# Kernel tuning notes

Hardware: AMD Instinct MI355X
Metric: run time of the kernel (lower is better)

## Reference

```python
import jax, jax.numpy as jnp
import numpy as np

N_TOKEN = 267735
D = 512           # d_embed == d_proj
DIV = 4
CUTS = [0, 20000, 40000, 200000, 267735]  # cutoff_ends
N_TOKENS_BATCH = 1024  # len*bsz


def setup_inputs() -> dict:
    key = jax.random.key(0)
    ks = jax.random.split(key, 16)
    inp = {}
    inp["hidden"] = jax.random.normal(ks[0], (N_TOKENS_BATCH, D), jnp.float32)
    inp["target"] = jax.random.randint(ks[1], (N_TOKENS_BATCH,), 0, N_TOKEN)
    d_embs = [D // DIV ** i for i in range(4)]          # 512, 128, 32, 8
    sizes = [CUTS[i + 1] - CUTS[i] for i in range(4)]   # 20000, 20000, 160000, 67735
    for i in range(4):
        inp[f"W{i}"] = jax.random.normal(ks[2 + 3 * i], (sizes[i], d_embs[i]), jnp.float32) * (d_embs[i] ** -0.5)
        inp[f"b{i}"] = jax.random.normal(ks[3 + 3 * i], (sizes[i],), jnp.float32) * 0.01
        inp[f"proj{i}"] = jax.random.normal(ks[4 + 3 * i], (D, d_embs[i]), jnp.float32) * (D ** -0.5)
    inp["cluster_weight"] = jax.random.normal(ks[14], (3, D), jnp.float32) * (D ** -0.5)
    inp["cluster_bias"] = jax.random.normal(ks[15], (3,), jnp.float32) * 0.01
    return inp


def reference(hidden, target, W0, b0, proj0, W1, b1, proj1, W2, b2, proj2, W3, b3, proj3, cluster_weight, cluster_bias):
    n = jnp.arange(target.shape[0])
    # head = shortlist vocab + one logit per tail cluster
    head_w = jnp.concatenate([W0, cluster_weight], axis=0)   # [20003, D]
    head_b = jnp.concatenate([b0, cluster_bias], axis=0)     # [20003]
    head_logit = (hidden @ proj0) @ head_w.T + head_b        # einsum('bd,de,ev->bv')
    head_lp = jax.nn.log_softmax(head_logit, axis=-1)        # [N, 20003]
    head_size = head_lp.shape[1]
    # cluster id per token (0 = shortlist, 1..3 = tails)
    cid = ((target >= CUTS[1]).astype(jnp.int32)
           + (target >= CUTS[2]).astype(jnp.int32)
           + (target >= CUTS[3]).astype(jnp.int32))
    # shortlist: nll = -head_logprob[n, target]
    nll = -head_lp[n, jnp.clip(target, 0, CUTS[1] - 1)]
    for i, (Wi, bi, pi) in enumerate([(W1, b1, proj1), (W2, b2, proj2), (W3, b3, proj3)], start=1):
        l, r = CUTS[i], CUTS[i + 1]
        tail_lp = jax.nn.log_softmax((hidden @ pi) @ Wi.T + bi, axis=-1)  # [N, r-l]
        rel = jnp.clip(target - l, 0, r - l - 1)
        # faithful to original: head column indexed as head_logprob[:, -i]
        lp_i = head_lp[:, head_size - i] + tail_lp[n, rel]
        nll = jnp.where(cid == i, -lp_i, nll)
    return nll
```

## Files before the change

kernel.cpp:

```cpp
#include <hip/hip_runtime.h>

typedef short s16x8 __attribute__((ext_vector_type(8)));
typedef unsigned short u16x8 __attribute__((ext_vector_type(8)));
typedef float f32x4 __attribute__((ext_vector_type(4)));
typedef unsigned short ushort;

#define NTOK 1024
#define DHID 512

#define VH   20003
#define KH   512
#define NCH_H 80
#define TPC_H 16
#define VH_PAD 20480

#define V1   20000
#define K1   128
#define NCH_1 80
#define TPC_1 16
#define V1_PAD 20480

#define V2   160000
#define K2   32
#define NCH_2 128
#define TPC_2 80
#define V2_PAD 163840

#define V3   67735
#define K3   32
#define NCH_3 67
#define TPC_3 64
#define V3_PAD 68608

#define PAD_BIAS (-1e30f)

#define OFF_HW   0UL
#define OFF_W1   (OFF_HW  + (unsigned long)VH_PAD*KH*2)
#define OFF_W2   (OFF_W1  + (unsigned long)V1_PAD*K1*2)
#define OFF_W3   (OFF_W2  + (unsigned long)V2_PAD*K2*2)
#define OFF_HID  (OFF_W3  + (unsigned long)V3_PAD*K3*2)
#define OFF_PT0  (OFF_HID + (unsigned long)NTOK*DHID*2)
#define OFF_PT1  (OFF_PT0 + (unsigned long)512*DHID*2)
#define OFF_PT2  (OFF_PT1 + (unsigned long)128*DHID*2)
#define OFF_PT3  (OFF_PT2 + (unsigned long)32*DHID*2)
#define OFF_H0   (OFF_PT3 + (unsigned long)32*DHID*2)
#define OFF_H1   (OFF_H0  + (unsigned long)NTOK*512*2)
#define OFF_H2   (OFF_H1  + (unsigned long)NTOK*128*2)
#define OFF_H3   (OFF_H2  + (unsigned long)NTOK*32*2)
#define OFF_HB   (OFF_H3  + (unsigned long)NTOK*32*2)
#define OFF_B1   (OFF_HB  + (unsigned long)VH_PAD*4)
#define OFF_B2   (OFF_B1  + (unsigned long)V1_PAD*4)
#define OFF_B3   (OFF_B2  + (unsigned long)V2_PAD*4)
#define OFF_SH   (OFF_B3  + (unsigned long)V3_PAD*4)
#define OFF_S1   (OFF_SH  + (unsigned long)NTOK*NCH_H*4)
#define OFF_S2   (OFF_S1  + (unsigned long)NTOK*NCH_1*4)
#define OFF_S3   (OFF_S2  + (unsigned long)NTOK*NCH_2*4)

__device__ __forceinline__ ushort f2bf(float f) {
    union { float f; unsigned u; } x; x.f = f;
    unsigned r = x.u + 0x7fffu + ((x.u >> 16) & 1u);
    return (ushort)(r >> 16);
}
__device__ __forceinline__ float bf2f(ushort h) {
    union { unsigned u; float f; } x; x.u = ((unsigned)h) << 16;
    return x.f;
}
__device__ __forceinline__ f32x4 mfma_bf16(s16x8 a, s16x8 b, f32x4 c) {
    return __builtin_amdgcn_mfma_f32_16x16x32_bf16(a, b, c, 0, 0, 0);
}
__device__ __forceinline__ void ld8(const float* p, float* v) {
    float4 a = *(const float4*)p, b = *(const float4*)(p + 4);
    v[0]=a.x; v[1]=a.y; v[2]=a.z; v[3]=a.w; v[4]=b.x; v[5]=b.y; v[6]=b.z; v[7]=b.w;
}

__device__ __forceinline__ void gld_lds16(const ushort* g, ushort* l) {
    __builtin_amdgcn_global_load_lds(
        (const __attribute__((address_space(1))) unsigned int*)g,
        (__attribute__((address_space(3))) unsigned int*)l, 16, 0, 0);
}

#define WB_HW  20480L
#define WB_W1  5120L
#define WB_W2  10240L
#define WB_W3  4288L
#define WB_HID 1024L
#define WB_PT0 512L
#define WB_PT1 128L
#define WB_PT2 32L
#define WB_PT3 32L
#define WB_TOTAL (WB_HW+WB_W1+WB_W2+WB_W3+WB_HID+WB_PT0+WB_PT1+WB_PT2+WB_PT3)

__global__ __launch_bounds__(256) void prep_wswz(
    const float* __restrict__ hidden,
    const float* __restrict__ W0, const float* __restrict__ cw,
    const float* __restrict__ W1, const float* __restrict__ W2, const float* __restrict__ W3,
    const float* __restrict__ p0, const float* __restrict__ p1,
    const float* __restrict__ p2, const float* __restrict__ p3,
    ushort* __restrict__ hw, ushort* __restrict__ ow1,
    ushort* __restrict__ ow2, ushort* __restrict__ ow3,
    ushort* __restrict__ hid,
    ushort* __restrict__ pT0, ushort* __restrict__ pT1,
    ushort* __restrict__ pT2, ushort* __restrict__ pT3)
{
    int lane = threadIdx.x & 63;
    int r = lane & 15, quad = lane >> 4;
    long wb0 = (long)blockIdx.x * 4 + (threadIdx.x >> 6);
    long nw = (long)gridDim.x * 4;
    for (long wb = wb0; wb < WB_TOTAL; wb += nw) {
        long b = wb;
        float vals[8];
        #pragma unroll
        for (int j = 0; j < 8; ++j) vals[j] = 0.f;
        ushort* dst;
        if (b < WB_HW) {
            long tile = b >> 4, ks = b & 15;
            long v = tile * 16 + r, k = ks * 32 + quad * 8;
            if (v < 20000)      ld8(W0 + v * 512 + k, vals);
            else if (v < VH)    ld8(cw + (v - 20000) * 512 + k, vals);
            dst = hw + b * 512 + (long)lane * 8;
        } else if ((b -= WB_HW) < WB_W1) {
            long tile = b >> 2, ks = b & 3;
            long v = tile * 16 + r, k = ks * 32 + quad * 8;
            if (v < V1) ld8(W1 + v * 128 + k, vals);
            dst = ow1 + b * 512 + (long)lane * 8;
        } else if ((b -= WB_W1) < WB_W2) {
            long v = b * 16 + r;
            if (v < V2) ld8(W2 + v * 32 + quad * 8, vals);
            dst = ow2 + b * 512 + (long)lane * 8;
        } else if ((b -= WB_W2) < WB_W3) {
            long v = b * 16 + r;
            if (v < V3 && quad == 0) ld8(W3 + v * 8, vals);
            dst = ow3 + b * 512 + (long)lane * 8;
        } else if ((b -= WB_W3) < WB_HID) {
            long tile = b >> 4, ks = b & 15;
            long v = tile * 16 + r, k = ks * 32 + quad * 8;
            ld8(hidden + v * 512 + k, vals);
            dst = hid + b * 512 + (long)lane * 8;
        } else if ((b -= WB_HID) < WB_PT0) {
            long tile = b >> 4, ks = b & 15;
            long c = tile * 16 + r, k = ks * 32 + quad * 8;
            #pragma unroll
            for (int j = 0; j < 8; ++j) vals[j] = p0[(k + j) * 512 + c];
            dst = pT0 + b * 512 + (long)lane * 8;
        } else if ((b -= WB_PT0) < WB_PT1) {
            long tile = b >> 4, ks = b & 15;
            long c = tile * 16 + r, k = ks * 32 + quad * 8;
            #pragma unroll
            for (int j = 0; j < 8; ++j) vals[j] = p1[(k + j) * 128 + c];
            dst = pT1 + b * 512 + (long)lane * 8;
        } else if ((b -= WB_PT1) < WB_PT2) {
            long tile = b >> 4, ks = b & 15;
            long c = tile * 16 + r, k = ks * 32 + quad * 8;
            #pragma unroll
            for (int j = 0; j < 8; ++j) vals[j] = p2[(k + j) * 32 + c];
            dst = pT2 + b * 512 + (long)lane * 8;
        } else {
            b -= WB_PT2;
            long tile = b >> 4, ks = b & 15;
            long c = tile * 16 + r, k = ks * 32 + quad * 8;
            if (c < 8) {
                #pragma unroll
                for (int j = 0; j < 8; ++j) vals[j] = p3[(k + j) * 8 + c];
            }
            dst = pT3 + b * 512 + (long)lane * 8;
        }
        u16x8 o;
        #pragma unroll
        for (int j = 0; j < 8; ++j) o[j] = f2bf(vals[j]);
        *(u16x8*)dst = o;
    }
}

#define E_HB  ((long)VH_PAD)
#define E_B1  ((long)V1_PAD)
#define E_B2  ((long)V2_PAD)
#define E_B3  ((long)V3_PAD)
#define E_BIAS (E_HB+E_B1+E_B2+E_B3)

__global__ __launch_bounds__(256) void prep_bias(
    const float* __restrict__ b0, const float* __restrict__ b1,
    const float* __restrict__ b2, const float* __restrict__ b3,
    const float* __restrict__ cb,
    float* __restrict__ hbp, float* __restrict__ ob1,
    float* __restrict__ ob2, float* __restrict__ ob3)
{
    long stride = (long)gridDim.x * blockDim.x;
    for (long i = (long)blockIdx.x * blockDim.x + threadIdx.x; i < E_BIAS; i += stride) {
        long j = i;
        if (j < E_HB) {
            hbp[j] = (j < 20000) ? b0[j] : (j < VH) ? cb[j - 20000] : PAD_BIAS;
        } else if ((j -= E_HB) < E_B1) {
            ob1[j] = (j < V1) ? b1[j] : PAD_BIAS;
        } else if ((j -= E_B1) < E_B2) {
            ob2[j] = (j < V2) ? b2[j] : PAD_BIAS;
        } else { j -= E_B2;
            ob3[j] = (j < V3) ? b3[j] : PAD_BIAS;
        }
    }
}

__global__ __launch_bounds__(256) void gemm_h(
    const ushort* __restrict__ A, const ushort* __restrict__ Bt,
    ushort* __restrict__ Hout, int dpad)
{
    int wave = threadIdx.x >> 6, lane = threadIdx.x & 63;
    int quad = lane >> 4, colid = lane & 15;
    int m_tile = blockIdx.x * 4 + wave;
    int c_tile = blockIdx.y;
    const ushort* Ab = A + ((long)m_tile * 16) * 512 + lane * 8;
    const ushort* Bb = Bt + ((long)c_tile * 16) * 512 + lane * 8;
    f32x4 acc = {0.f, 0.f, 0.f, 0.f};
    #pragma unroll
    for (int ks = 0; ks < 16; ++ks) {
        s16x8 a = *(const s16x8*)(Ab + ks * 512);
        s16x8 b = *(const s16x8*)(Bb + ks * 512);
        acc = mfma_bf16(a, b, acc);
    }
    int KBo = dpad >> 5;
    int col = c_tile * 16 + colid;
    int ks_o = col >> 5, q_o = (col >> 3) & 3, j_o = col & 7;
    #pragma unroll
    for (int r = 0; r < 4; ++r) {
        int rm = quad * 4 + r;
        Hout[((long)m_tile * KBo + ks_o) * 512 + (q_o * 16 + rm) * 8 + j_o] = f2bf(acc[r]);
    }
}


template<int TG>
__device__ __forceinline__ void stage_grp(const ushort* __restrict__ gsrc_base,
                                          ushort* __restrict__ buf,
                                          int wave, int lane)
{
    constexpr int LPW = TG / 4;
    const ushort* g = gsrc_base + ((long)wave * LPW) * 512 + lane * 8;
    ushort* l = buf + (wave * LPW) * 512;
    #pragma unroll
    for (int i = 0; i < LPW; ++i)
        gld_lds16(g + i * 512, l + i * 512);
}

template<int KB, int TG>
__device__ __forceinline__ void compute_grp(const ushort* __restrict__ buf,
                                            const s16x8 (&afrag)[KB],
                                            const float* __restrict__ bias,
                                            long tile0, int lane, int colid,
                                            float (&s_acc)[4])
{
    constexpr int TPG = TG / KB;
    f32x4 acc0[TPG], acc1[TPG];
    #pragma unroll
    for (int t = 0; t < TPG; ++t) {
        acc0[t] = (f32x4){0.f, 0.f, 0.f, 0.f};
        acc1[t] = (f32x4){0.f, 0.f, 0.f, 0.f};
    }
    #pragma unroll
    for (int b = 0; b < TG; ++b) {
        s16x8 bb = *(const s16x8*)(buf + b * 512 + lane * 8);
        int t = b / KB, ks = b % KB;
        if ((KB > 1) && (ks & 1))
            acc1[t] = mfma_bf16(afrag[ks], bb, acc1[t]);
        else
            acc0[t] = mfma_bf16(afrag[ks], bb, acc0[t]);
    }
    #pragma unroll
    for (int t = 0; t < TPG; ++t) {
        float bval = bias[(tile0 + t) * 16 + colid];
        #pragma unroll
        for (int r = 0; r < 4; ++r) {
            float v = acc0[t][r];
            if (KB > 1) v += acc1[t][r];
            s_acc[r] += __expf(v + bval);
        }
    }
}

template<int KB, int TG>
__global__ __launch_bounds__(256, 4) void fused_lse_lds(
    const ushort* __restrict__ A, const ushort* __restrict__ W,
    const float* __restrict__ bias, float* __restrict__ part_s,
    int tpc, int n_chunks)
{
    constexpr int TPG = TG / KB;
    __shared__ __align__(16) ushort lds0[TG * 512];
    __shared__ __align__(16) ushort lds1[TG * 512];

    int wave = threadIdx.x >> 6, lane = threadIdx.x & 63;
    int quad = lane >> 4, colid = lane & 15;
    int m_tile = blockIdx.x * 4 + wave;
    long t0 = (long)blockIdx.y * tpc;
    const ushort* Wc = W + t0 * KB * 512;

    s16x8 afrag[KB];
    const ushort* Ab = A + ((long)m_tile * KB) * 512 + lane * 8;
    #pragma unroll
    for (int ks = 0; ks < KB; ++ks) afrag[ks] = *(const s16x8*)(Ab + ks * 512);

    const int ng = (tpc * KB) / TG;
    float s_acc[4] = {0.f, 0.f, 0.f, 0.f};

    stage_grp<TG>(Wc, lds0, wave, lane);
    asm volatile("s_waitcnt vmcnt(0)" ::: "memory");
    __syncthreads();

    for (int g = 0; g < ng; g += 2) {
        if (g + 1 < ng)
            stage_grp<TG>(Wc + ((long)(g + 1) * TG) * 512, lds1, wave, lane);
        compute_grp<KB, TG>(lds0, afrag, bias, t0 + (long)g * TPG, lane, colid, s_acc);
        asm volatile("s_waitcnt vmcnt(0)" ::: "memory");
        __syncthreads();

        if (g + 2 < ng)
            stage_grp<TG>(Wc + ((long)(g + 2) * TG) * 512, lds0, wave, lane);
        if (g + 1 < ng) {
            compute_grp<KB, TG>(lds1, afrag, bias, t0 + (long)(g + 1) * TPG, lane, colid, s_acc);
            asm volatile("s_waitcnt vmcnt(0)" ::: "memory");
            __syncthreads();
        }
    }

    #pragma unroll
    for (int r = 0; r < 4; ++r) {
        float v = s_acc[r];
        v += __shfl_xor(v, 1);
        v += __shfl_xor(v, 2);
        v += __shfl_xor(v, 4);
        v += __shfl_xor(v, 8);
        s_acc[r] = v;
    }
    if (colid == 0) {
        #pragma unroll
        for (int r = 0; r < 4; ++r) {
            int m = m_tile * 16 + quad * 4 + r;
            part_s[(long)m * n_chunks + blockIdx.y] = s_acc[r];
        }
    }
}

__device__ __forceinline__ float swz_dot(const ushort* __restrict__ H, int m,
                                         const ushort* __restrict__ Wm, long vrow,
                                         int K, int lane)
{
    float d = 0.f;
    if (lane * 8 < K) {
        int ks = lane >> 2, q = lane & 3;
        int KB = K >> 5;
        const ushort* hp = H + ((long)(m >> 4) * KB + ks) * 512 + (q * 16 + (m & 15)) * 8;
        const ushort* wp = Wm + ((vrow >> 4) * KB + ks) * 512 + (q * 16 + (int)(vrow & 15)) * 8;
        #pragma unroll
        for (int j = 0; j < 8; ++j) d += bf2f(hp[j]) * bf2f(wp[j]);
    }
    d += __shfl_xor(d, 1);  d += __shfl_xor(d, 2);  d += __shfl_xor(d, 4);
    d += __shfl_xor(d, 8);  d += __shfl_xor(d, 16); d += __shfl_xor(d, 32);
    return d;
}

__global__ __launch_bounds__(256) void finalize_kernel(
    const int* __restrict__ target,
    const ushort* __restrict__ H0, const ushort* __restrict__ hw,
    const float* __restrict__ hbp, const float* __restrict__ sH,
    const ushort* __restrict__ H1, const ushort* __restrict__ w1,
    const float* __restrict__ b1p, const float* __restrict__ s1,
    const ushort* __restrict__ H2, const ushort* __restrict__ w2,
    const float* __restrict__ b2p, const float* __restrict__ s2,
    const ushort* __restrict__ H3, const ushort* __restrict__ w3,
    const float* __restrict__ b3p, const float* __restrict__ s3,
    float* __restrict__ out)
{
    int wave = threadIdx.x >> 6, lane = threadIdx.x & 63;
    int m = blockIdx.x * 4 + wave;
    int t = target[m];
    int cid = (t >= 20000) + (t >= 40000) + (t >= 200000);

    float s = 0.f;
    for (int i = lane; i < NCH_H; i += 64) s += sH[(long)m * NCH_H + i];
    s += __shfl_xor(s, 1);  s += __shfl_xor(s, 2);  s += __shfl_xor(s, 4);
    s += __shfl_xor(s, 8);  s += __shfl_xor(s, 16); s += __shfl_xor(s, 32);
    float lse_h = __logf(s);

    int hc = (cid == 0) ? t : (20003 - cid);
    float d = swz_dot(H0, m, hw, hc, 512, lane);
    float nll = lse_h - (d + hbp[hc]);

    if (cid > 0) {
        const ushort *Hi, *Wi; const float *bi, *si; int K, nc, l;
        if (cid == 1)      { Hi = H1; Wi = w1; bi = b1p; si = s1; K = 128; nc = NCH_1; l = 20000; }
        else if (cid == 2) { Hi = H2; Wi = w2; bi = b2p; si = s2; K = 32;  nc = NCH_2; l = 40000; }
        else               { Hi = H3; Wi = w3; bi = b3p; si = s3; K = 32;  nc = NCH_3; l = 200000; }
        int rel = t - l;
        float ts = 0.f;
        for (int i = lane; i < nc; i += 64) ts += si[(long)m * nc + i];
        ts += __shfl_xor(ts, 1);  ts += __shfl_xor(ts, 2);  ts += __shfl_xor(ts, 4);
        ts += __shfl_xor(ts, 8);  ts += __shfl_xor(ts, 16); ts += __shfl_xor(ts, 32);
        float lse_t = __logf(ts);
        float dt = swz_dot(Hi, m, Wi, rel, K, lane);
        nll += lse_t - (dt + bi[rel]);
    }
    if (lane == 0) out[m] = nll;
}

extern "C" void kernel_launch(void* const* d_in, const int* in_sizes, int n_in,
                              void* d_out, int out_size, void* d_ws, size_t ws_size,
                              hipStream_t stream) {
    const float* hidden = (const float*)d_in[0];
    const int*   target = (const int*)d_in[1];
    const float* W0 = (const float*)d_in[2];
    const float* b0 = (const float*)d_in[3];
    const float* p0 = (const float*)d_in[4];
    const float* W1 = (const float*)d_in[5];
    const float* b1 = (const float*)d_in[6];
    const float* p1 = (const float*)d_in[7];
    const float* W2 = (const float*)d_in[8];
    const float* b2 = (const float*)d_in[9];
    const float* p2 = (const float*)d_in[10];
    const float* W3 = (const float*)d_in[11];
    const float* b3 = (const float*)d_in[12];
    const float* p3 = (const float*)d_in[13];
    const float* cw = (const float*)d_in[14];
    const float* cb = (const float*)d_in[15];

    char* ws = (char*)d_ws;
    ushort* hw  = (ushort*)(ws + OFF_HW);
    ushort* ow1 = (ushort*)(ws + OFF_W1);
    ushort* ow2 = (ushort*)(ws + OFF_W2);
    ushort* ow3 = (ushort*)(ws + OFF_W3);
    ushort* hid = (ushort*)(ws + OFF_HID);
    ushort* pT0 = (ushort*)(ws + OFF_PT0);
    ushort* pT1 = (ushort*)(ws + OFF_PT1);
    ushort* pT2 = (ushort*)(ws + OFF_PT2);
    ushort* pT3 = (ushort*)(ws + OFF_PT3);
    ushort* H0  = (ushort*)(ws + OFF_H0);
    ushort* H1  = (ushort*)(ws + OFF_H1);
    ushort* H2  = (ushort*)(ws + OFF_H2);
    ushort* H3  = (ushort*)(ws + OFF_H3);
    float* hbp = (float*)(ws + OFF_HB);
    float* b1p = (float*)(ws + OFF_B1);
    float* b2p = (float*)(ws + OFF_B2);
    float* b3p = (float*)(ws + OFF_B3);
    float* sH  = (float*)(ws + OFF_SH);
    float* s1  = (float*)(ws + OFF_S1);
    float* s2  = (float*)(ws + OFF_S2);
    float* s3  = (float*)(ws + OFF_S3);

    prep_wswz<<<10464, 256, 0, stream>>>(hidden, W0, cw, W1, W2, W3,
                                         p0, p1, p2, p3,
                                         hw, ow1, ow2, ow3, hid, pT0, pT1, pT2, pT3);
    prep_bias<<<1072, 256, 0, stream>>>(b0, b1, b2, b3, cb, hbp, b1p, b2p, b3p);

    gemm_h<<<dim3(NTOK / 64, 512 / 16), 256, 0, stream>>>(hid, pT0, H0, 512);
    gemm_h<<<dim3(NTOK / 64, 128 / 16), 256, 0, stream>>>(hid, pT1, H1, 128);
    gemm_h<<<dim3(NTOK / 64, 32 / 16),  256, 0, stream>>>(hid, pT2, H2, 32);
    gemm_h<<<dim3(NTOK / 64, 32 / 16),  256, 0, stream>>>(hid, pT3, H3, 32);

    fused_lse_lds<16, 16><<<dim3(NTOK / 64, NCH_H), 256, 0, stream>>>(H0, hw,  hbp, sH, TPC_H, NCH_H);
    fused_lse_lds<4, 8><<<dim3(NTOK / 64, NCH_1), 256, 0, stream>>>(H1, ow1, b1p, s1, TPC_1, NCH_1);
    fused_lse_lds<1, 8><<<dim3(NTOK / 64, NCH_2), 256, 0, stream>>>(H2, ow2, b2p, s2, TPC_2, NCH_2);
    fused_lse_lds<1, 8><<<dim3(NTOK / 64, NCH_3), 256, 0, stream>>>(H3, ow3, b3p, s3, TPC_3, NCH_3);

    finalize_kernel<<<NTOK / 4, 256, 0, stream>>>(target,
        H0, hw, hbp, sH, H1, ow1, b1p, s1, H2, ow2, b2p, s2, H3, ow3, b3p, s3,
        (float*)d_out);
}
```

Before: 261.9 us.

## Merge per-cluster GEMM and LSE launches and triple-buffer weight staging

Combines the four projection GEMM launches into one kernel dispatched by blockIdx.y, and the four fused logsumexp launches into one flat-grid kernel whose block index is remapped so blocks sharing a weight chunk run close together. The LSE loop moves from a double buffer with full vmcnt(0) waits to a three-deep LDS ring using partial vmcnt waits and raw barriers. Biases are staged into LDS, and occupancy hint drops to 3 blocks. This targets launch overhead, tail effects between small kernels, and load/compute overlap, at the cost of more LDS per block, possible lower occupancy, and fragile manual waitcnt ordering.

```diff
diff --git a/kernel.cpp b/kernel.cpp
--- a/kernel.cpp
+++ b/kernel.cpp
@@ -72,7 +72,6 @@
     float4 a = *(const float4*)p, b = *(const float4*)(p + 4);
     v[0]=a.x; v[1]=a.y; v[2]=a.z; v[3]=a.w; v[4]=b.x; v[5]=b.y; v[6]=b.z; v[7]=b.w;
 }
-
 __device__ __forceinline__ void gld_lds16(const ushort* g, ushort* l) {
     __builtin_amdgcn_global_load_lds(
         (const __attribute__((address_space(1))) unsigned int*)g,
@@ -199,14 +198,13 @@
     }
 }
 
-__global__ __launch_bounds__(256) void gemm_h(
+__device__ __forceinline__ void gemm_body(
     const ushort* __restrict__ A, const ushort* __restrict__ Bt,
-    ushort* __restrict__ Hout, int dpad)
+    ushort* __restrict__ Hout, int dpad, int c_tile)
 {
     int wave = threadIdx.x >> 6, lane = threadIdx.x & 63;
     int quad = lane >> 4, colid = lane & 15;
     int m_tile = blockIdx.x * 4 + wave;
-    int c_tile = blockIdx.y;
     const ushort* Ab = A + ((long)m_tile * 16) * 512 + lane * 8;
     const ushort* Bb = Bt + ((long)c_tile * 16) * 512 + lane * 8;
     f32x4 acc = {0.f, 0.f, 0.f, 0.f};
@@ -226,28 +224,39 @@
     }
 }
 
-
-template<int TG>
-__device__ __forceinline__ void stage_grp(const ushort* __restrict__ gsrc_base,
-                                          ushort* __restrict__ buf,
-                                          int wave, int lane)
-{
-    constexpr int LPW = TG / 4;
-    const ushort* g = gsrc_base + ((long)wave * LPW) * 512 + lane * 8;
-    ushort* l = buf + (wave * LPW) * 512;
-    #pragma unroll
-    for (int i = 0; i < LPW; ++i)
-        gld_lds16(g + i * 512, l + i * 512);
-}
-
-template<int KB, int TG>
-__device__ __forceinline__ void compute_grp(const ushort* __restrict__ buf,
-                                            const s16x8 (&afrag)[KB],
-                                            const float* __restrict__ bias,
-                                            long tile0, int lane, int colid,
-                                            float (&s_acc)[4])
-{
-    constexpr int TPG = TG / KB;
+__global__ __launch_bounds__(256) void gemm_all(
+    const ushort* __restrict__ hid,
+    const ushort* __restrict__ pT0, const ushort* __restrict__ pT1,
+    const ushort* __restrict__ pT2, const ushort* __restrict__ pT3,
+    ushort* __restrict__ H0, ushort* __restrict__ H1,
+    ushort* __restrict__ H2, ushort* __restrict__ H3)
+{
+    int y = blockIdx.y;
+    if (y < 32)      gemm_body(hid, pT0, H0, 512, y);
+    else if (y < 40) gemm_body(hid, pT1, H1, 128, y - 32);
+    else if (y < 42) gemm_body(hid, pT2, H2, 32,  y - 40);
+    else             gemm_body(hid, pT3, H3, 32,  y - 42);
+}
+
+
+__device__ __forceinline__ void stage_grp16(const ushort* __restrict__ g,
+                                            ushort* __restrict__ l,
+                                            int wave, int lane)
+{
+    const ushort* gp = g + ((long)wave * 4) * 512 + lane * 8;
+    ushort* lp = l + wave * 4 * 512;
+    #pragma unroll
+    for (int i = 0; i < 4; ++i) gld_lds16(gp + i * 512, lp + i * 512);
+}
+
+template<int KB>
+__device__ __forceinline__ void compute_grp16(const ushort* __restrict__ buf,
+                                              const s16x8 (&afrag)[KB],
+                                              const float* __restrict__ ldsB,
+                                              int tb0, int lane, int colid,
+                                              float (&s_acc)[4])
+{
+    constexpr int TPG = 16 / KB;
     f32x4 acc0[TPG], acc1[TPG];
     #pragma unroll
     for (int t = 0; t < TPG; ++t) {
@@ -255,7 +264,7 @@
         acc1[t] = (f32x4){0.f, 0.f, 0.f, 0.f};
     }
     #pragma unroll
-    for (int b = 0; b < TG; ++b) {
+    for (int b = 0; b < 16; ++b) {
         s16x8 bb = *(const s16x8*)(buf + b * 512 + lane * 8);
         int t = b / KB, ks = b % KB;
         if ((KB > 1) && (ks & 1))
@@ -265,7 +274,7 @@
     }
     #pragma unroll
     for (int t = 0; t < TPG; ++t) {
-        float bval = bias[(tile0 + t) * 16 + colid];
+        float bval = ldsB[(tb0 + t) * 16 + colid];
         #pragma unroll
         for (int r = 0; r < 4; ++r) {
             float v = acc0[t][r];
@@ -275,49 +284,55 @@
     }
 }
 
-template<int KB, int TG>
-__global__ __launch_bounds__(256, 4) void fused_lse_lds(
-    const ushort* __restrict__ A, const ushort* __restrict__ W,
-    const float* __restrict__ bias, float* __restrict__ part_s,
-    int tpc, int n_chunks)
-{
-    constexpr int TPG = TG / KB;
-    __shared__ __align__(16) ushort lds0[TG * 512];
-    __shared__ __align__(16) ushort lds1[TG * 512];
-
+template<int KB>
+__device__ __forceinline__ void fused_path(const ushort* __restrict__ A,
+                                           const ushort* __restrict__ W,
+                                           const float* __restrict__ bias,
+                                           float* __restrict__ part_s,
+                                           int tpc, int n_chunks, int chunk, int mblk,
+                                           ushort* __restrict__ ldsW,
+                                           float* __restrict__ ldsB)
+{
+    constexpr int TPG = 16 / KB;
     int wave = threadIdx.x >> 6, lane = threadIdx.x & 63;
     int quad = lane >> 4, colid = lane & 15;
-    int m_tile = blockIdx.x * 4 + wave;
-    long t0 = (long)blockIdx.y * tpc;
+    int m_tile = mblk * 4 + wave;
+    long t0 = (long)chunk * tpc;
     const ushort* Wc = W + t0 * KB * 512;
+    int ng = (tpc * KB) >> 4;
 
     s16x8 afrag[KB];
     const ushort* Ab = A + ((long)m_tile * KB) * 512 + lane * 8;
     #pragma unroll
     for (int ks = 0; ks < KB; ++ks) afrag[ks] = *(const s16x8*)(Ab + ks * 512);
 
-    const int ng = (tpc * KB) / TG;
+    int nb = tpc * 16;
+    for (int i = threadIdx.x; i < nb; i += 256) ldsB[i] = bias[t0 * 16 + i];
+    __syncthreads();
+    #pragma unroll
+    for (int ks = 0; ks < KB; ++ks) asm volatile("" : "+v"(afrag[ks]));
+
     float s_acc[4] = {0.f, 0.f, 0.f, 0.f};
 
-    stage_grp<TG>(Wc, lds0, wave, lane);
+    stage_grp16(Wc, ldsW, wave, lane);
+    stage_grp16(Wc + 16 * 512, ldsW + 16 * 512, wave, lane);
+
+    for (int g = 0; g < ng - 1; ++g) {
+        asm volatile("s_waitcnt vmcnt(4)" ::: "memory");
+        __builtin_amdgcn_s_barrier();
+        asm volatile("" ::: "memory");
+        if (g + 2 < ng)
+            stage_grp16(Wc + (long)(g + 2) * 16 * 512,
+                        ldsW + ((g + 2) % 3) * (16 * 512), wave, lane);
+        compute_grp16<KB>(ldsW + (g % 3) * (16 * 512), afrag, ldsB,
+                          g * TPG, lane, colid, s_acc);
+        asm volatile("s_waitcnt lgkmcnt(0)" ::: "memory");
+    }
     asm volatile("s_waitcnt vmcnt(0)" ::: "memory");
-    __syncthreads();
-
-    for (int g = 0; g < ng; g += 2) {
-        if (g + 1 < ng)
-            stage_grp<TG>(Wc + ((long)(g + 1) * TG) * 512, lds1, wave, lane);
-        compute_grp<KB, TG>(lds0, afrag, bias, t0 + (long)g * TPG, lane, colid, s_acc);
-        asm volatile("s_waitcnt vmcnt(0)" ::: "memory");
-        __syncthreads();
-
-        if (g + 2 < ng)
-            stage_grp<TG>(Wc + ((long)(g + 2) * TG) * 512, lds0, wave, lane);
-        if (g + 1 < ng) {
-            compute_grp<KB, TG>(lds1, afrag, bias, t0 + (long)(g + 1) * TPG, lane, colid, s_acc);
-            asm volatile("s_waitcnt vmcnt(0)" ::: "memory");
-            __syncthreads();
-        }
-    }
+    __builtin_amdgcn_s_barrier();
+    asm volatile("" ::: "memory");
+    compute_grp16<KB>(ldsW + ((ng - 1) % 3) * (16 * 512), afrag, ldsB,
+                      (ng - 1) * TPG, lane, colid, s_acc);
 
     #pragma unroll
     for (int r = 0; r < 4; ++r) {
@@ -332,9 +347,32 @@
         #pragma unroll
         for (int r = 0; r < 4; ++r) {
             int m = m_tile * 16 + quad * 4 + r;
-            part_s[(long)m * n_chunks + blockIdx.y] = s_acc[r];
+            part_s[(long)m * n_chunks + chunk] = s_acc[r];
         }
     }
+}
+
+__global__ __launch_bounds__(256, 3) void fused_all(
+    const ushort* __restrict__ H0, const ushort* __restrict__ hw,
+    const float* __restrict__ hbp, float* __restrict__ sH,
+    const ushort* __restrict__ H1, const ushort* __restrict__ w1,
+    const float* __restrict__ b1p, float* __restrict__ s1,
+    const ushort* __restrict__ H2, const ushort* __restrict__ w2,
+    const float* __restrict__ b2p, float* __restrict__ s2,
+    const ushort* __restrict__ H3, const ushort* __restrict__ w3,
+    const float* __restrict__ b3p, float* __restrict__ s3)
+{
+    __shared__ __align__(16) ushort ldsW[3 * 16 * 512];
+    __shared__ float ldsB[1280];
+    int id = blockIdx.x;
+    int k = id & 7, s = id >> 3;
+    int c = (s >> 4) * 8 + k;
+    int mblk = s & 15;
+    if (c >= 355) return;
+    if (c < 80)       fused_path<16>(H0, hw, hbp, sH, TPC_H, NCH_H, c,       mblk, ldsW, ldsB);
+    else if (c < 160) fused_path<4>(H1, w1, b1p, s1, TPC_1, NCH_1, c - 80,  mblk, ldsW, ldsB);
+    else if (c < 288) fused_path<1>(H2, w2, b2p, s2, TPC_2, NCH_2, c - 160, mblk, ldsW, ldsB);
+    else              fused_path<1>(H3, w3, b3p, s3, TPC_3, NCH_3, c - 288, mblk, ldsW, ldsB);
 }
 
 __device__ __forceinline__ float swz_dot(const ushort* __restrict__ H, int m,
@@ -447,15 +485,13 @@
                                          hw, ow1, ow2, ow3, hid, pT0, pT1, pT2, pT3);
     prep_bias<<<1072, 256, 0, stream>>>(b0, b1, b2, b3, cb, hbp, b1p, b2p, b3p);
 
-    gemm_h<<<dim3(NTOK / 64, 512 / 16), 256, 0, stream>>>(hid, pT0, H0, 512);
-    gemm_h<<<dim3(NTOK / 64, 128 / 16), 256, 0, stream>>>(hid, pT1, H1, 128);
-    gemm_h<<<dim3(NTOK / 64, 32 / 16),  256, 0, stream>>>(hid, pT2, H2, 32);
-    gemm_h<<<dim3(NTOK / 64, 32 / 16),  256, 0, stream>>>(hid, pT3, H3, 32);
-
-    fused_lse_lds<16, 16><<<dim3(NTOK / 64, NCH_H), 256, 0, stream>>>(H0, hw,  hbp, sH, TPC_H, NCH_H);
-    fused_lse_lds<4, 8><<<dim3(NTOK / 64, NCH_1), 256, 0, stream>>>(H1, ow1, b1p, s1, TPC_1, NCH_1);
-    fused_lse_lds<1, 8><<<dim3(NTOK / 64, NCH_2), 256, 0, stream>>>(H2, ow2, b2p, s2, TPC_2, NCH_2);
-    fused_lse_lds<1, 8><<<dim3(NTOK / 64, NCH_3), 256, 0, stream>>>(H3, ow3, b3p, s3, TPC_3, NCH_3);
+    gemm_all<<<dim3(NTOK / 64, 44), 256, 0, stream>>>(hid, pT0, pT1, pT2, pT3,
+                                                      H0, H1, H2, H3);
+
+    fused_all<<<5760, 256, 0, stream>>>(H0, hw, hbp, sH,
+                                        H1, ow1, b1p, s1,
+                                        H2, ow2, b2p, s2,
+                                        H3, ow3, b3p, s3);
 
     finalize_kernel<<<NTOK / 4, 256, 0, stream>>>(target,
         H0, hw, hbp, sH, H1, ow1, b1p, s1, H2, ow2, b2p, s2, H3, ow3, b3p, s3,
```

New measurement: 254.0 us. 3.0% less time.
